# Kernel tuning notes

Measured on AMD Instinct MI355X. Metric: run time of the kernel, lower is better.

Reference implementation:

```python
import jax, jax.numpy as jnp
import numpy as np

B, S = 32, 128
VIDEO_SIZE, TITLE_SIZE = 768, 768
NUM_TAG, NUM_VOCAB, HIDDEN = 10000, 21128, 256


def setup_inputs() -> dict:
    key = jax.random.key(0)
    ks = jax.random.split(key, 10)
    video_feature = jax.random.normal(ks[0], (B, VIDEO_SIZE), dtype=jnp.float32)
    title_feature = jax.random.normal(ks[1], (B, S, TITLE_SIZE), dtype=jnp.float32)
    label_tag = jax.random.uniform(ks[2], (B, NUM_TAG), dtype=jnp.float32)
    label_mlm = jax.random.randint(ks[3], (B, S), 0, NUM_VOCAB, dtype=jnp.int64)
    Wt = jax.random.normal(ks[4], (NUM_TAG, VIDEO_SIZE), dtype=jnp.float32) * 0.02
    bt = jnp.zeros((NUM_TAG,), dtype=jnp.float32)
    Wm = jax.random.normal(ks[5], (NUM_VOCAB, TITLE_SIZE), dtype=jnp.float32) * 0.02
    bm = jnp.zeros((NUM_VOCAB,), dtype=jnp.float32)
    Wh = jax.random.normal(ks[6], (HIDDEN, VIDEO_SIZE + TITLE_SIZE), dtype=jnp.float32) * 0.02
    bh = jnp.zeros((HIDDEN,), dtype=jnp.float32)
    return {
        "video_feature": video_feature,
        "title_feature": title_feature,
        "label_tag": label_tag,
        "label_mlm": label_mlm,
        "Wt": Wt, "bt": bt, "Wm": Wm, "bm": bm, "Wh": Wh, "bh": bh,
    }


def reference(video_feature, title_feature, label_tag, label_mlm, Wt, bt, Wm, bm, Wh, bh):
    # tag head + BCEWithLogits (mean reduction), numerically stable form
    pred_tag = video_feature @ Wt.T + bt                       # [B, NUM_TAG]
    loss_tag = jnp.mean(
        jnp.maximum(pred_tag, 0.0) - pred_tag * label_tag
        + jnp.log1p(jnp.exp(-jnp.abs(pred_tag)))
    )
    pred_tag_sig = jax.nn.sigmoid(pred_tag)

    # mlm head: per-token vocab logits, masked CE summed over nonzero labels
    logits = jnp.einsum('bsd,vd->bsv', title_feature, Wm) + bm  # [B, S, V]
    lse = jax.nn.logsumexp(logits, axis=-1)                     # [B, S]
    gold = jnp.take_along_axis(logits, label_mlm[..., None], axis=-1)[..., 0]
    ce = lse - gold                                             # per-token NLL
    mask = (label_mlm != 0)
    loss_mlm = jnp.sum(jnp.where(mask, ce, 0.0))

    # fused embedding head + L2 normalize (torch eps 1e-12)
    feature = jnp.concatenate([video_feature, title_feature[:, 0]], axis=1)
    embedding = feature @ Wh.T + bh                             # [B, HIDDEN]
    norm = jnp.linalg.norm(embedding, axis=1, keepdims=True)
    normed_embedding = embedding / jnp.maximum(norm, 1e-12)

    return (pred_tag_sig, normed_embedding, loss_tag, loss_mlm)
```

## Files before the change

kernel.cpp:

```cpp
#include <hip/hip_runtime.h>
#include <hip/hip_bf16.h>
#include <math.h>

typedef short bf16x8 __attribute__((ext_vector_type(8)));
typedef float f32x4 __attribute__((ext_vector_type(4)));

#define KDIM 768
#define NTAG 10000
#define NVOC 21128
#define HID 256
#define NTOK 4096
#define NCHUNK 24
#define CHUNK 881
#define NTILE 28
#define TILEB 24576
#define M0 4.0f
#define WMSCALE 16.0f
#define INVSCALE 0.0625f
#define LOG2E 1.44269504f

#define WS_A     0ull
#define WS_PSUM  3145728ull
#define WS_GOLD  3538944ull
#define WS_TAGL  3555328ull
#define WS_WM8   3555392ull
#define WS_NEED  (WS_WM8 + 16515072ull + 65536ull)

#define OUT_EMB  320000
#define OUT_LTAG 328192
#define OUT_LMLM 328193

#define MLM_BLKS 768
#define TAG_BLKS 313
#define GOLD_BLKS 1024
#define EMB_BLKS 32
#define CONV_BLKS 1536
#define WMCV_BLKS (NCHUNK*NTILE)
#define TAIL_BLKS (TAG_BLKS + GOLD_BLKS + EMB_BLKS)

typedef const __attribute__((address_space(1))) unsigned int glds_g;
typedef __attribute__((address_space(3))) unsigned int glds_l;

static __device__ __forceinline__ unsigned short f2bf(float f) {
  unsigned u = __builtin_bit_cast(unsigned, f);
  u = u + 0x7FFFu + ((u >> 16) & 1u);
  return (unsigned short)(u >> 16);
}

static __device__ __forceinline__ int pk4_fp8(float4 v, float scale) {
  int w = __builtin_amdgcn_cvt_pk_fp8_f32(v.x * scale, v.y * scale, 0, false);
  w = __builtin_amdgcn_cvt_pk_fp8_f32(v.z * scale, v.w * scale, w, true);
  return w;
}

__global__ __launch_bounds__(256) void k_pre(
    const float* __restrict__ title, const float* __restrict__ video,
    const float* __restrict__ Wm,
    const float* __restrict__ Wt, const float* __restrict__ bt,
    const float* __restrict__ ylab, const int* __restrict__ lab,
    const float* __restrict__ bm,
    const float* __restrict__ Wh, const float* __restrict__ bh,
    char* __restrict__ A8, char* __restrict__ Wm8,
    float* __restrict__ out_sig, float* __restrict__ tagSum,
    float* __restrict__ gold, float* __restrict__ out_emb) {
  __shared__ __align__(1024) char smem[49664];
  const int bid = blockIdx.x, tid = threadIdx.x;
  const int wave = tid >> 6, lane = tid & 63, g = lane >> 4, col16 = lane & 15;

  if (bid < TAG_BLKS) {
    unsigned short* Bt = (unsigned short*)smem;
    float* wsum = (float*)(smem + 49152);
    #pragma unroll
    for (int j = 0; j < 12; ++j) {
      int sg = j * 256 + tid;
      int tt = (j >= 6) ? 1 : 0;
      int sgl = sg - tt * 1536;
      int kk = sgl >> 6, c = (sgl & 63) >> 2, gg = sgl & 3;
      int n = (bid * 2 + tt) * 16 + c;
      bf16x8 o = {};
      if (n < NTAG) {
        const float* wp = Wt + (size_t)n * KDIM + kk * 32 + gg * 8;
        float4 f0 = ((const float4*)wp)[0], f1 = ((const float4*)wp)[1];
        o[0] = (short)f2bf(f0.x); o[1] = (short)f2bf(f0.y);
        o[2] = (short)f2bf(f0.z); o[3] = (short)f2bf(f0.w);
        o[4] = (short)f2bf(f1.x); o[5] = (short)f2bf(f1.y);
        o[6] = (short)f2bf(f1.z); o[7] = (short)f2bf(f1.w);
      }
      *(bf16x8*)((char*)Bt + sg * 16) = o;
    }
    __syncthreads();

    const int ntile = bid * 2 + (wave >> 1), mhalf = wave & 1;
    float lacc = 0.f;
    if (ntile < 625) {
      bf16x8 a[24];
      const float* vrow = video + (size_t)(mhalf * 16 + col16) * KDIM;
      #pragma unroll
      for (int kk = 0; kk < 24; ++kk) {
        float4 f0 = *(const float4*)(vrow + kk * 32 + g * 8);
        float4 f1 = *(const float4*)(vrow + kk * 32 + g * 8 + 4);
        bf16x8 o;
        o[0] = (short)f2bf(f0.x); o[1] = (short)f2bf(f0.y);
        o[2] = (short)f2bf(f0.z); o[3] = (short)f2bf(f0.w);
        o[4] = (short)f2bf(f1.x); o[5] = (short)f2bf(f1.y);
        o[6] = (short)f2bf(f1.z); o[7] = (short)f2bf(f1.w);
        a[kk] = o;
      }
      const char* Bb = (const char*)Bt + (wave >> 1) * 24576 + col16 * 64 + g * 16;
      f32x4 acc = {0.f, 0.f, 0.f, 0.f};
      #pragma unroll
      for (int kk = 0; kk < 24; ++kk) {
        bf16x8 b = *(const bf16x8*)(Bb + kk * 1024);
        acc = __builtin_amdgcn_mfma_f32_16x16x32_bf16(a[kk], b, acc, 0, 0, 0);
      }
      const int nc = ntile * 16 + col16;
      if (nc < NTAG) {
        const float bias = bt[nc];
        #pragma unroll
        for (int rr = 0; rr < 4; ++rr) {
          int brow = mhalf * 16 + g * 4 + rr;
          float x = acc[rr] + bias;
          out_sig[(size_t)brow * NTAG + nc] = 1.f / (1.f + __expf(-x));
          float y = ylab[(size_t)brow * NTAG + nc];
          lacc += fmaxf(x, 0.f) - x * y + log1pf(__expf(-fabsf(x)));
        }
      }
    }
    #pragma unroll
    for (int m = 32; m; m >>= 1) lacc += __shfl_xor(lacc, m);
    if (lane == 0) wsum[wave] = lacc;
    __syncthreads();
    if (tid == 0) atomicAdd(tagSum, wsum[0] + wsum[1] + wsum[2] + wsum[3]);

  } else if (bid < TAG_BLKS + GOLD_BLKS) {
    int tok = (bid - TAG_BLKS) * 4 + wave;
    int l = lab[tok];
    float acc = 0.f;
    #pragma unroll
    for (int j = 0; j < 12; ++j) {
      int k = j * 64 + lane;
      acc += title[(size_t)tok * KDIM + k] * Wm[(size_t)l * KDIM + k];
    }
    #pragma unroll
    for (int m = 32; m; m >>= 1) acc += __shfl_xor(acc, m);
    if (lane == 0) gold[tok] = acc + bm[l];

  } else if (bid < TAIL_BLKS) {
    float* feat = (float*)smem;
    float* red = (float*)(smem + 49152);
    const int b = bid - TAG_BLKS - GOLD_BLKS;
    #pragma unroll
    for (int j = 0; j < 6; ++j) {
      int k = j * 256 + tid;
      feat[k] = (k < KDIM) ? video[(size_t)b * KDIM + k]
                           : title[(size_t)b * 128 * KDIM + (k - KDIM)];
    }
    __syncthreads();
    float acc = bh[tid];
    #pragma unroll 8
    for (int k = 0; k < 1536; k += 4) {
      float4 w = *(const float4*)(Wh + (size_t)tid * 1536 + k);
      acc += w.x * feat[k] + w.y * feat[k + 1] + w.z * feat[k + 2] + w.w * feat[k + 3];
    }
    float ss = acc * acc;
    #pragma unroll
    for (int m = 32; m; m >>= 1) ss += __shfl_xor(ss, m);
    if (lane == 0) red[wave] = ss;
    __syncthreads();
    float nrm = sqrtf(red[0] + red[1] + red[2] + red[3]);
    float scale = 1.f / fmaxf(nrm, 1e-12f);
    out_emb[(size_t)b * HID + tid] = acc * scale;

  } else if (bid < TAIL_BLKS + CONV_BLKS) {
    int i = (bid - TAIL_BLKS) * 256 + tid;
    float4 v0 = ((const float4*)title)[i * 2];
    float4 v1 = ((const float4*)title)[i * 2 + 1];
    int2 o = {pk4_fp8(v0, 1.f), pk4_fp8(v1, 1.f)};
    *(int2*)(A8 + (size_t)i * 8) = o;

  } else {
    char* tsm = smem;
    const int wblk = bid - TAIL_BLKS - CONV_BLKS;
    const int chunk = wblk / NTILE, tile = wblk % NTILE;
    const int n0 = chunk * CHUNK + tile * 32;
    const int nend = min(chunk * CHUNK + CHUNK, NVOC);
    #pragma unroll
    for (int j = 0; j < 12; ++j) {
      int p = j * 256 + tid;
      int r = p / 96, q = p % 96;
      int n = n0 + r;
      int2 o = {0, 0};
      if (n < nend) {
        const float* wp = Wm + (size_t)n * KDIM + q * 8;
        o.x = pk4_fp8(((const float4*)wp)[0], WMSCALE);
        o.y = pk4_fp8(((const float4*)wp)[1], WMSCALE);
      }
      *(int2*)(tsm + (q >> 2) * 1024 + (q & 3) * 256 + r * 8) = o;
    }
    __syncthreads();
    char* dst = Wm8 + (size_t)wblk * TILEB;
    #pragma unroll
    for (int j = 0; j < 6; ++j) {
      int idx = j * 256 + tid;
      *(int4*)(dst + idx * 16) = *(const int4*)(tsm + idx * 16);
    }
  }
}

template<bool WM8>
__global__ __launch_bounds__(256)
__attribute__((amdgpu_waves_per_eu(3, 3)))
void k_mlm(
    const char* __restrict__ A8,
    const float* __restrict__ Wm,
    const char* __restrict__ Wm8,
    const float* __restrict__ bm,
    float* __restrict__ psum) {
  __shared__ __align__(1024) char smem[2 * TILEB + 3584];
  char (*Bsm)[TILEB] = (char(*)[TILEB])smem;
  float* biasS = (float*)(smem + 2 * TILEB);
  const int tid = threadIdx.x;
  const int wave = tid >> 6, lane = tid & 63, g = lane >> 4, col = lane & 15;
  const int chunk = blockIdx.x % NCHUNK, mt = blockIdx.x / NCHUNK;
  const int nbeg = chunk * CHUNK;
  const int nend = min(nbeg + CHUNK, NVOC);

  for (int i = tid; i < NTILE * 32; i += 256) {
    int n = nbeg + i;
    biasS[i] = (n < nend) ? (bm[n] - M0) * LOG2E : -1e30f;
  }

  const int arow0 = mt * 128 + wave * 32;
  long a0[24], a1[24];
  #pragma unroll
  for (int kk = 0; kk < 24; ++kk) {
    a0[kk] = *(const long*)(A8 + (size_t)(arow0 + col) * KDIM + kk * 32 + g * 8);
    a1[kk] = *(const long*)(A8 + (size_t)(arow0 + 16 + col) * KDIM + kk * 32 + g * 8);
  }

  float s[8];
  #pragma unroll
  for (int i = 0; i < 8; ++i) s[i] = 0.f;

  const int off0 = col * 8 + g * 256;
  const float kinv = INVSCALE * LOG2E;

  auto COMPUTE = [&](int t) {
    const char* B = &Bsm[t & 1][0] + off0;
    f32x4 acc00 = {0.f,0.f,0.f,0.f}, acc10 = {0.f,0.f,0.f,0.f};
    f32x4 acc01 = {0.f,0.f,0.f,0.f}, acc11 = {0.f,0.f,0.f,0.f};
    #pragma unroll
    for (int kk = 0; kk < 24; ++kk) {
      long b0 = *(const long*)(B + kk * 1024);
      long b1 = *(const long*)(B + kk * 1024 + 128);
      acc00 = __builtin_amdgcn_mfma_f32_16x16x32_fp8_fp8(a0[kk], b0, acc00, 0, 0, 0);
      acc10 = __builtin_amdgcn_mfma_f32_16x16x32_fp8_fp8(a1[kk], b0, acc10, 0, 0, 0);
      acc01 = __builtin_amdgcn_mfma_f32_16x16x32_fp8_fp8(a0[kk], b1, acc01, 0, 0, 0);
      acc11 = __builtin_amdgcn_mfma_f32_16x16x32_fp8_fp8(a1[kk], b1, acc11, 0, 0, 0);
    }
    const float b20 = biasS[t * 32 + col];
    const float b21 = biasS[t * 32 + 16 + col];
    #pragma unroll
    for (int rr = 0; rr < 4; ++rr) {
      s[rr]     += exp2f(fmaf(acc00[rr], kinv, b20)) + exp2f(fmaf(acc01[rr], kinv, b21));
      s[rr + 4] += exp2f(fmaf(acc10[rr], kinv, b20)) + exp2f(fmaf(acc11[rr], kinv, b21));
    }
  };

  if constexpr (WM8) {
    const char* cbase = Wm8 + (size_t)chunk * NTILE * TILEB;
    auto STAGE = [&](int buf, int tt) {
      const char* src = cbase + (size_t)tt * TILEB + wave * 1024 + lane * 16;
      char* dst = &Bsm[buf][0] + wave * 1024;
      #pragma unroll
      for (int j = 0; j < 6; ++j) {
        __builtin_amdgcn_global_load_lds((glds_g*)(src + j * 4096),
                                         (glds_l*)(dst + j * 4096), 16, 0, 0);
      }
    };
    STAGE(0, 0);
    asm volatile("s_waitcnt lgkmcnt(0)" ::: "memory");
    __builtin_amdgcn_s_barrier();
    for (int t = 0; t < NTILE; ++t) {
      int tn = (t + 1 < NTILE) ? t + 1 : 0;
      STAGE((t + 1) & 1, tn);
      asm volatile("s_waitcnt vmcnt(6)" ::: "memory");
      __builtin_amdgcn_s_barrier();
      __builtin_amdgcn_sched_barrier(0);
      __builtin_amdgcn_s_setprio(1);
      COMPUTE(t);
      __builtin_amdgcn_s_setprio(0);
      __builtin_amdgcn_sched_barrier(0);
      __builtin_amdgcn_s_barrier();
    }
  } else {
    __syncthreads();
    for (int t = 0; t < NTILE; ++t) {
      #pragma unroll
      for (int j = 0; j < 6; ++j) {
        int sg = j * 256 + tid;
        int kk = sg >> 6, gg = (sg >> 4) & 3, nl0 = (sg & 15) * 2;
        int n_a = nbeg + t * 32 + nl0, n_b = n_a + 1;
        int4 o = {0, 0, 0, 0};
        if (n_a < nend) {
          const float* wp = Wm + (size_t)n_a * KDIM + kk * 32 + gg * 8;
          o.x = pk4_fp8(((const float4*)wp)[0], WMSCALE);
          o.y = pk4_fp8(((const float4*)wp)[1], WMSCALE);
        }
        if (n_b < nend) {
          const float* wp = Wm + (size_t)n_b * KDIM + kk * 32 + gg * 8;
          o.z = pk4_fp8(((const float4*)wp)[0], WMSCALE);
          o.w = pk4_fp8(((const float4*)wp)[1], WMSCALE);
        }
        *(int4*)(&Bsm[0][0] + kk * 1024 + gg * 256 + nl0 * 8) = o;
      }
      __syncthreads();
      COMPUTE(t);
      __syncthreads();
    }
  }

  #pragma unroll
  for (int i = 0; i < 8; ++i) {
    float v = s[i];
    v += __shfl_xor(v, 1);
    v += __shfl_xor(v, 2);
    v += __shfl_xor(v, 4);
    v += __shfl_xor(v, 8);
    s[i] = v;
  }
  if (col == 0) {
    #pragma unroll
    for (int mblk = 0; mblk < 2; ++mblk)
      #pragma unroll
      for (int rr = 0; rr < 4; ++rr) {
        int tok = arow0 + mblk * 16 + g * 4 + rr;
        psum[tok * NCHUNK + chunk] = s[mblk * 4 + rr];
      }
  }
}

__global__ __launch_bounds__(256) void k_final(
    const float* __restrict__ psum, const float* __restrict__ gold,
    const int* __restrict__ lab, const float* __restrict__ tagSum,
    float* __restrict__ out) {
  __shared__ float red[4];
  const int tid = threadIdx.x, wave = tid >> 6, lane = tid & 63;
  if (tid == 0) out[OUT_LTAG] = tagSum[0] / 320000.f;

  float lm = 0.f;
  for (int tok = tid; tok < NTOK; tok += 256) {
    float S = 0.f;
    #pragma unroll
    for (int c = 0; c < NCHUNK; ++c) S += psum[tok * NCHUNK + c];
    float lse = M0 + logf(S);
    if (lab[tok] != 0) lm += lse - gold[tok];
  }
  #pragma unroll
  for (int m = 32; m; m >>= 1) lm += __shfl_xor(lm, m);
  if (lane == 0) red[wave] = lm;
  __syncthreads();
  if (tid == 0) out[OUT_LMLM] = red[0] + red[1] + red[2] + red[3];
}

extern "C" void kernel_launch(void* const* d_in, const int* in_sizes, int n_in,
                              void* d_out, int out_size, void* d_ws, size_t ws_size,
                              hipStream_t stream) {
  const float* video = (const float*)d_in[0];
  const float* title = (const float*)d_in[1];
  const float* ylab  = (const float*)d_in[2];
  const int*   lab   = (const int*)d_in[3];
  const float* Wt = (const float*)d_in[4];
  const float* bt = (const float*)d_in[5];
  const float* Wm = (const float*)d_in[6];
  const float* bm = (const float*)d_in[7];
  const float* Wh = (const float*)d_in[8];
  const float* bh = (const float*)d_in[9];
  float* out = (float*)d_out;
  char* ws = (char*)d_ws;

  char* wsA8   = ws + WS_A;
  float* wsPsum = (float*)(ws + WS_PSUM);
  float* wsGold = (float*)(ws + WS_GOLD);
  float* wsTagl = (float*)(ws + WS_TAGL);
  char* wsWm8  = ws + WS_WM8;

  const bool useWm8 = ws_size >= WS_NEED;

  hipMemsetAsync(wsTagl, 0, 4, stream);
  k_pre<<<TAIL_BLKS + CONV_BLKS + WMCV_BLKS, 256, 0, stream>>>(
      title, video, Wm, Wt, bt, ylab, lab, bm, Wh, bh,
      wsA8, wsWm8, out, wsTagl, wsGold, out + OUT_EMB);
  if (useWm8)
    k_mlm<true><<<MLM_BLKS, 256, 0, stream>>>(wsA8, Wm, wsWm8, bm, wsPsum);
  else
    k_mlm<false><<<MLM_BLKS, 256, 0, stream>>>(wsA8, Wm, wsWm8, bm, wsPsum);
  k_final<<<1, 256, 0, stream>>>(wsPsum, wsGold, lab, wsTagl, out);
}
```

Baseline: 184.9 us.

## Overlap tag, gold and embedding heads with MLM GEMM in one interleaved kernel

Splits the prep kernel so that only the fp8 conversions of title and Wm run first, then merges the tag head, gold-logit gather and embedding head into the MLM kernel. Blocks are interleaved by role (3 of every 8 do MLM, 5 do tail work) so the independent small heads fill CUs alongside the long-running MLM blocks. It also makes the gold blocks process 16 tokens each instead of 4. The trade-off is a larger grid with many early-exit blocks. The shared-memory footprint and the waves-per-eu constraint now apply to the tail work too, which could limit how many blocks fit on a CU at once.

```diff
diff --git a/kernel.cpp b/kernel.cpp
--- a/kernel.cpp
+++ b/kernel.cpp
@@ -32,11 +32,12 @@
 
 #define MLM_BLKS 768
 #define TAG_BLKS 313
-#define GOLD_BLKS 1024
+#define GOLD_BLKS 256
 #define EMB_BLKS 32
+#define TAIL_JOBS (TAG_BLKS + GOLD_BLKS + EMB_BLKS)
+#define MAIN_GRID 2048
 #define CONV_BLKS 1536
 #define WMCV_BLKS (NCHUNK*NTILE)
-#define TAIL_BLKS (TAG_BLKS + GOLD_BLKS + EMB_BLKS)
 
 typedef const __attribute__((address_space(1))) unsigned int glds_g;
 typedef __attribute__((address_space(3))) unsigned int glds_l;
@@ -53,21 +54,194 @@
   return w;
 }
 
-__global__ __launch_bounds__(256) void k_pre(
-    const float* __restrict__ title, const float* __restrict__ video,
+__global__ __launch_bounds__(256) void k_conv(
+    const float* __restrict__ title, const float* __restrict__ Wm,
+    char* __restrict__ A8, char* __restrict__ Wm8) {
+  __shared__ __align__(1024) char tsm[TILEB];
+  const int bid = blockIdx.x, tid = threadIdx.x;
+  if (bid < CONV_BLKS) {
+    int i = bid * 256 + tid;
+    float4 v0 = ((const float4*)title)[i * 2];
+    float4 v1 = ((const float4*)title)[i * 2 + 1];
+    int2 o = {pk4_fp8(v0, 1.f), pk4_fp8(v1, 1.f)};
+    *(int2*)(A8 + (size_t)i * 8) = o;
+  } else {
+    const int wblk = bid - CONV_BLKS;
+    const int chunk = wblk / NTILE, tile = wblk % NTILE;
+    const int n0 = chunk * CHUNK + tile * 32;
+    const int nend = min(chunk * CHUNK + CHUNK, NVOC);
+    #pragma unroll
+    for (int j = 0; j < 12; ++j) {
+      int p = j * 256 + tid;
+      int r = p / 96, q = p % 96;
+      int n = n0 + r;
+      int2 o = {0, 0};
+      if (n < nend) {
+        const float* wp = Wm + (size_t)n * KDIM + q * 8;
+        o.x = pk4_fp8(((const float4*)wp)[0], WMSCALE);
+        o.y = pk4_fp8(((const float4*)wp)[1], WMSCALE);
+      }
+      *(int2*)(tsm + (q >> 2) * 1024 + (q & 3) * 256 + r * 8) = o;
+    }
+    __syncthreads();
+    char* dst = Wm8 + (size_t)wblk * TILEB;
+    #pragma unroll
+    for (int j = 0; j < 6; ++j) {
+      int idx = j * 256 + tid;
+      *(int4*)(dst + idx * 16) = *(const int4*)(tsm + idx * 16);
+    }
+  }
+}
+
+template<bool WM8>
+__global__ __launch_bounds__(256)
+__attribute__((amdgpu_waves_per_eu(3, 3)))
+void k_main(
+    const char* __restrict__ A8,
     const float* __restrict__ Wm,
+    const char* __restrict__ Wm8,
+    const float* __restrict__ bm,
+    float* __restrict__ psum,
+    const float* __restrict__ video, const float* __restrict__ title,
     const float* __restrict__ Wt, const float* __restrict__ bt,
     const float* __restrict__ ylab, const int* __restrict__ lab,
-    const float* __restrict__ bm,
     const float* __restrict__ Wh, const float* __restrict__ bh,
-    char* __restrict__ A8, char* __restrict__ Wm8,
     float* __restrict__ out_sig, float* __restrict__ tagSum,
     float* __restrict__ gold, float* __restrict__ out_emb) {
-  __shared__ __align__(1024) char smem[49664];
+  __shared__ __align__(1024) char smem[2 * TILEB + 3584];
   const int bid = blockIdx.x, tid = threadIdx.x;
-  const int wave = tid >> 6, lane = tid & 63, g = lane >> 4, col16 = lane & 15;
-
-  if (bid < TAG_BLKS) {
+  const int wave = tid >> 6, lane = tid & 63, g = lane >> 4, col = lane & 15;
+  const int role = bid & 7;
+
+  if (role < 3) {
+    const int mlm_idx = (bid >> 3) * 3 + role;
+    char (*Bsm)[TILEB] = (char(*)[TILEB])smem;
+    float* biasS = (float*)(smem + 2 * TILEB);
+    const int chunk = mlm_idx % NCHUNK, mt = mlm_idx / NCHUNK;
+    const int nbeg = chunk * CHUNK;
+    const int nend = min(nbeg + CHUNK, NVOC);
+
+    for (int i = tid; i < NTILE * 32; i += 256) {
+      int n = nbeg + i;
+      biasS[i] = (n < nend) ? (bm[n] - M0) * LOG2E : -1e30f;
+    }
+
+    const int arow0 = mt * 128 + wave * 32;
+    long a0[24], a1[24];
+    #pragma unroll
+    for (int kk = 0; kk < 24; ++kk) {
+      a0[kk] = *(const long*)(A8 + (size_t)(arow0 + col) * KDIM + kk * 32 + g * 8);
+      a1[kk] = *(const long*)(A8 + (size_t)(arow0 + 16 + col) * KDIM + kk * 32 + g * 8);
+    }
+
+    float s[8];
+    #pragma unroll
+    for (int i = 0; i < 8; ++i) s[i] = 0.f;
+
+    const int off0 = col * 8 + g * 256;
+    const float kinv = INVSCALE * LOG2E;
+
+    auto COMPUTE = [&](int t) {
+      const char* B = &Bsm[t & 1][0] + off0;
+      f32x4 acc00 = {0.f,0.f,0.f,0.f}, acc10 = {0.f,0.f,0.f,0.f};
+      f32x4 acc01 = {0.f,0.f,0.f,0.f}, acc11 = {0.f,0.f,0.f,0.f};
+      #pragma unroll
+      for (int kk = 0; kk < 24; ++kk) {
+        long b0 = *(const long*)(B + kk * 1024);
+        long b1 = *(const long*)(B + kk * 1024 + 128);
+        acc00 = __builtin_amdgcn_mfma_f32_16x16x32_fp8_fp8(a0[kk], b0, acc00, 0, 0, 0);
+        acc10 = __builtin_amdgcn_mfma_f32_16x16x32_fp8_fp8(a1[kk], b0, acc10, 0, 0, 0);
+        acc01 = __builtin_amdgcn_mfma_f32_16x16x32_fp8_fp8(a0[kk], b1, acc01, 0, 0, 0);
+        acc11 = __builtin_amdgcn_mfma_f32_16x16x32_fp8_fp8(a1[kk], b1, acc11, 0, 0, 0);
+      }
+      const float b20 = biasS[t * 32 + col];
+      const float b21 = biasS[t * 32 + 16 + col];
+      #pragma unroll
+      for (int rr = 0; rr < 4; ++rr) {
+        s[rr]     += exp2f(fmaf(acc00[rr], kinv, b20)) + exp2f(fmaf(acc01[rr], kinv, b21));
+        s[rr + 4] += exp2f(fmaf(acc10[rr], kinv, b20)) + exp2f(fmaf(acc11[rr], kinv, b21));
+      }
+    };
+
+    if constexpr (WM8) {
+      const char* cbase = Wm8 + (size_t)chunk * NTILE * TILEB;
+      auto STAGE = [&](int buf, int tt) {
+        const char* src = cbase + (size_t)tt * TILEB + wave * 1024 + lane * 16;
+        char* dst = &Bsm[buf][0] + wave * 1024;
+        #pragma unroll
+        for (int j = 0; j < 6; ++j) {
+          __builtin_amdgcn_global_load_lds((glds_g*)(src + j * 4096),
+                                           (glds_l*)(dst + j * 4096), 16, 0, 0);
+        }
+      };
+      STAGE(0, 0);
+      asm volatile("s_waitcnt lgkmcnt(0)" ::: "memory");
+      __builtin_amdgcn_s_barrier();
+      for (int t = 0; t < NTILE; ++t) {
+        int tn = (t + 1 < NTILE) ? t + 1 : 0;
+        STAGE((t + 1) & 1, tn);
+        asm volatile("s_waitcnt vmcnt(6)" ::: "memory");
+        __builtin_amdgcn_s_barrier();
+        __builtin_amdgcn_sched_barrier(0);
+        __builtin_amdgcn_s_setprio(1);
+        COMPUTE(t);
+        __builtin_amdgcn_s_setprio(0);
+        __builtin_amdgcn_sched_barrier(0);
+        __builtin_amdgcn_s_barrier();
+      }
+    } else {
+      __syncthreads();
+      for (int t = 0; t < NTILE; ++t) {
+        #pragma unroll
+        for (int j = 0; j < 6; ++j) {
+          int sg = j * 256 + tid;
+          int kk = sg >> 6, gg = (sg >> 4) & 3, nl0 = (sg & 15) * 2;
+          int n_a = nbeg + t * 32 + nl0, n_b = n_a + 1;
+          int4 o = {0, 0, 0, 0};
+          if (n_a < nend) {
+            const float* wp = Wm + (size_t)n_a * KDIM + kk * 32 + gg * 8;
+            o.x = pk4_fp8(((const float4*)wp)[0], WMSCALE);
+            o.y = pk4_fp8(((const float4*)wp)[1], WMSCALE);
+          }
+          if (n_b < nend) {
+            const float* wp = Wm + (size_t)n_b * KDIM + kk * 32 + gg * 8;
+            o.z = pk4_fp8(((const float4*)wp)[0], WMSCALE);
+            o.w = pk4_fp8(((const float4*)wp)[1], WMSCALE);
+          }
+          *(int4*)(&Bsm[0][0] + kk * 1024 + gg * 256 + nl0 * 8) = o;
+        }
+        __syncthreads();
+        COMPUTE(t);
+        __syncthreads();
+      }
+    }
+
+    #pragma unroll
+    for (int i = 0; i < 8; ++i) {
+      float v = s[i];
+      v += __shfl_xor(v, 1);
+      v += __shfl_xor(v, 2);
+      v += __shfl_xor(v, 4);
+      v += __shfl_xor(v, 8);
+      s[i] = v;
+    }
+    if (col == 0) {
+      #pragma unroll
+      for (int mblk = 0; mblk < 2; ++mblk)
+        #pragma unroll
+        for (int rr = 0; rr < 4; ++rr) {
+          int tok = arow0 + mblk * 16 + g * 4 + rr;
+          psum[tok * NCHUNK + chunk] = s[mblk * 4 + rr];
+        }
+    }
+    return;
+  }
+
+  const int tail_idx = (bid >> 3) * 5 + (role - 3);
+  if (tail_idx >= TAIL_JOBS) return;
+
+  if (tail_idx < TAG_BLKS) {
+    const int tb = tail_idx;
     unsigned short* Bt = (unsigned short*)smem;
     float* wsum = (float*)(smem + 49152);
     #pragma unroll
@@ -76,7 +250,7 @@
       int tt = (j >= 6) ? 1 : 0;
       int sgl = sg - tt * 1536;
       int kk = sgl >> 6, c = (sgl & 63) >> 2, gg = sgl & 3;
-      int n = (bid * 2 + tt) * 16 + c;
+      int n = (tb * 2 + tt) * 16 + c;
       bf16x8 o = {};
       if (n < NTAG) {
         const float* wp = Wt + (size_t)n * KDIM + kk * 32 + gg * 8;
@@ -90,11 +264,11 @@
     }
     __syncthreads();
 
-    const int ntile = bid * 2 + (wave >> 1), mhalf = wave & 1;
+    const int ntile = tb * 2 + (wave >> 1), mhalf = wave & 1;
     float lacc = 0.f;
     if (ntile < 625) {
       bf16x8 a[24];
-      const float* vrow = video + (size_t)(mhalf * 16 + col16) * KDIM;
+      const float* vrow = video + (size_t)(mhalf * 16 + col) * KDIM;
       #pragma unroll
       for (int kk = 0; kk < 24; ++kk) {
         float4 f0 = *(const float4*)(vrow + kk * 32 + g * 8);
@@ -106,14 +280,14 @@
         o[6] = (short)f2bf(f1.z); o[7] = (short)f2bf(f1.w);
         a[kk] = o;
       }
-      const char* Bb = (const char*)Bt + (wave >> 1) * 24576 + col16 * 64 + g * 16;
+      const char* Bb = (const char*)Bt + (wave >> 1) * 24576 + col * 64 + g * 16;
       f32x4 acc = {0.f, 0.f, 0.f, 0.f};
       #pragma unroll
       for (int kk = 0; kk < 24; ++kk) {
         bf16x8 b = *(const bf16x8*)(Bb + kk * 1024);
         acc = __builtin_amdgcn_mfma_f32_16x16x32_bf16(a[kk], b, acc, 0, 0, 0);
       }
-      const int nc = ntile * 16 + col16;
+      const int nc = ntile * 16 + col;
       if (nc < NTAG) {
         const float bias = bt[nc];
         #pragma unroll
@@ -132,23 +306,27 @@
     __syncthreads();
     if (tid == 0) atomicAdd(tagSum, wsum[0] + wsum[1] + wsum[2] + wsum[3]);
 
-  } else if (bid < TAG_BLKS + GOLD_BLKS) {
-    int tok = (bid - TAG_BLKS) * 4 + wave;
-    int l = lab[tok];
-    float acc = 0.f;
-    #pragma unroll
-    for (int j = 0; j < 12; ++j) {
-      int k = j * 64 + lane;
-      acc += title[(size_t)tok * KDIM + k] * Wm[(size_t)l * KDIM + k];
-    }
-    #pragma unroll
-    for (int m = 32; m; m >>= 1) acc += __shfl_xor(acc, m);
-    if (lane == 0) gold[tok] = acc + bm[l];
-
-  } else if (bid < TAIL_BLKS) {
+  } else if (tail_idx < TAG_BLKS + GOLD_BLKS) {
+    const int tbase = (tail_idx - TAG_BLKS) * 16;
+    #pragma unroll
+    for (int u = 0; u < 4; ++u) {
+      int tok = tbase + wave * 4 + u;
+      int l = lab[tok];
+      float acc = 0.f;
+      #pragma unroll
+      for (int j = 0; j < 12; ++j) {
+        int k = j * 64 + lane;
+        acc += title[(size_t)tok * KDIM + k] * Wm[(size_t)l * KDIM + k];
+      }
+      #pragma unroll
+      for (int m = 32; m; m >>= 1) acc += __shfl_xor(acc, m);
+      if (lane == 0) gold[tok] = acc + bm[l];
+    }
+
+  } else {
     float* feat = (float*)smem;
     float* red = (float*)(smem + 49152);
-    const int b = bid - TAG_BLKS - GOLD_BLKS;
+    const int b = tail_idx - TAG_BLKS - GOLD_BLKS;
     #pragma unroll
     for (int j = 0; j < 6; ++j) {
       int k = j * 256 + tid;
@@ -170,173 +348,6 @@
     float nrm = sqrtf(red[0] + red[1] + red[2] + red[3]);
     float scale = 1.f / fmaxf(nrm, 1e-12f);
     out_emb[(size_t)b * HID + tid] = acc * scale;
-
-  } else if (bid < TAIL_BLKS + CONV_BLKS) {
-    int i = (bid - TAIL_BLKS) * 256 + tid;
-    float4 v0 = ((const float4*)title)[i * 2];
-    float4 v1 = ((const float4*)title)[i * 2 + 1];
-    int2 o = {pk4_fp8(v0, 1.f), pk4_fp8(v1, 1.f)};
-    *(int2*)(A8 + (size_t)i * 8) = o;
-
-  } else {
-    char* tsm = smem;
-    const int wblk = bid - TAIL_BLKS - CONV_BLKS;
-    const int chunk = wblk / NTILE, tile = wblk % NTILE;
-    const int n0 = chunk * CHUNK + tile * 32;
-    const int nend = min(chunk * CHUNK + CHUNK, NVOC);
-    #pragma unroll
-    for (int j = 0; j < 12; ++j) {
-      int p = j * 256 + tid;
-      int r = p / 96, q = p % 96;
-      int n = n0 + r;
-      int2 o = {0, 0};
-      if (n < nend) {
-        const float* wp = Wm + (size_t)n * KDIM + q * 8;
-        o.x = pk4_fp8(((const float4*)wp)[0], WMSCALE);
-        o.y = pk4_fp8(((const float4*)wp)[1], WMSCALE);
-      }
-      *(int2*)(tsm + (q >> 2) * 1024 + (q & 3) * 256 + r * 8) = o;
-    }
-    __syncthreads();
-    char* dst = Wm8 + (size_t)wblk * TILEB;
-    #pragma unroll
-    for (int j = 0; j < 6; ++j) {
-      int idx = j * 256 + tid;
-      *(int4*)(dst + idx * 16) = *(const int4*)(tsm + idx * 16);
-    }
-  }
-}
-
-template<bool WM8>
-__global__ __launch_bounds__(256)
-__attribute__((amdgpu_waves_per_eu(3, 3)))
-void k_mlm(
-    const char* __restrict__ A8,
-    const float* __restrict__ Wm,
-    const char* __restrict__ Wm8,
-    const float* __restrict__ bm,
-    float* __restrict__ psum) {
-  __shared__ __align__(1024) char smem[2 * TILEB + 3584];
-  char (*Bsm)[TILEB] = (char(*)[TILEB])smem;
-  float* biasS = (float*)(smem + 2 * TILEB);
-  const int tid = threadIdx.x;
-  const int wave = tid >> 6, lane = tid & 63, g = lane >> 4, col = lane & 15;
-  const int chunk = blockIdx.x % NCHUNK, mt = blockIdx.x / NCHUNK;
-  const int nbeg = chunk * CHUNK;
-  const int nend = min(nbeg + CHUNK, NVOC);
-
-  for (int i = tid; i < NTILE * 32; i += 256) {
-    int n = nbeg + i;
-    biasS[i] = (n < nend) ? (bm[n] - M0) * LOG2E : -1e30f;
-  }
-
-  const int arow0 = mt * 128 + wave * 32;
-  long a0[24], a1[24];
-  #pragma unroll
-  for (int kk = 0; kk < 24; ++kk) {
-    a0[kk] = *(const long*)(A8 + (size_t)(arow0 + col) * KDIM + kk * 32 + g * 8);
-    a1[kk] = *(const long*)(A8 + (size_t)(arow0 + 16 + col) * KDIM + kk * 32 + g * 8);
-  }
-
-  float s[8];
-  #pragma unroll
-  for (int i = 0; i < 8; ++i) s[i] = 0.f;
-
-  const int off0 = col * 8 + g * 256;
-  const float kinv = INVSCALE * LOG2E;
-
-  auto COMPUTE = [&](int t) {
-    const char* B = &Bsm[t & 1][0] + off0;
-    f32x4 acc00 = {0.f,0.f,0.f,0.f}, acc10 = {0.f,0.f,0.f,0.f};
-    f32x4 acc01 = {0.f,0.f,0.f,0.f}, acc11 = {0.f,0.f,0.f,0.f};
-    #pragma unroll
-    for (int kk = 0; kk < 24; ++kk) {
-      long b0 = *(const long*)(B + kk * 1024);
-      long b1 = *(const long*)(B + kk * 1024 + 128);
-      acc00 = __builtin_amdgcn_mfma_f32_16x16x32_fp8_fp8(a0[kk], b0, acc00, 0, 0, 0);
-      acc10 = __builtin_amdgcn_mfma_f32_16x16x32_fp8_fp8(a1[kk], b0, acc10, 0, 0, 0);
-      acc01 = __builtin_amdgcn_mfma_f32_16x16x32_fp8_fp8(a0[kk], b1, acc01, 0, 0, 0);
-      acc11 = __builtin_amdgcn_mfma_f32_16x16x32_fp8_fp8(a1[kk], b1, acc11, 0, 0, 0);
-    }
-    const float b20 = biasS[t * 32 + col];
-    const float b21 = biasS[t * 32 + 16 + col];
-    #pragma unroll
-    for (int rr = 0; rr < 4; ++rr) {
-      s[rr]     += exp2f(fmaf(acc00[rr], kinv, b20)) + exp2f(fmaf(acc01[rr], kinv, b21));
-      s[rr + 4] += exp2f(fmaf(acc10[rr], kinv, b20)) + exp2f(fmaf(acc11[rr], kinv, b21));
-    }
-  };
-
-  if constexpr (WM8) {
-    const char* cbase = Wm8 + (size_t)chunk * NTILE * TILEB;
-    auto STAGE = [&](int buf, int tt) {
-      const char* src = cbase + (size_t)tt * TILEB + wave * 1024 + lane * 16;
-      char* dst = &Bsm[buf][0] + wave * 1024;
-      #pragma unroll
-      for (int j = 0; j < 6; ++j) {
-        __builtin_amdgcn_global_load_lds((glds_g*)(src + j * 4096),
-                                         (glds_l*)(dst + j * 4096), 16, 0, 0);
-      }
-    };
-    STAGE(0, 0);
-    asm volatile("s_waitcnt lgkmcnt(0)" ::: "memory");
-    __builtin_amdgcn_s_barrier();
-    for (int t = 0; t < NTILE; ++t) {
-      int tn = (t + 1 < NTILE) ? t + 1 : 0;
-      STAGE((t + 1) & 1, tn);
-      asm volatile("s_waitcnt vmcnt(6)" ::: "memory");
-      __builtin_amdgcn_s_barrier();
-      __builtin_amdgcn_sched_barrier(0);
-      __builtin_amdgcn_s_setprio(1);
-      COMPUTE(t);
-      __builtin_amdgcn_s_setprio(0);
-      __builtin_amdgcn_sched_barrier(0);
-      __builtin_amdgcn_s_barrier();
-    }
-  } else {
-    __syncthreads();
-    for (int t = 0; t < NTILE; ++t) {
-      #pragma unroll
-      for (int j = 0; j < 6; ++j) {
-        int sg = j * 256 + tid;
-        int kk = sg >> 6, gg = (sg >> 4) & 3, nl0 = (sg & 15) * 2;
-        int n_a = nbeg + t * 32 + nl0, n_b = n_a + 1;
-        int4 o = {0, 0, 0, 0};
-        if (n_a < nend) {
-          const float* wp = Wm + (size_t)n_a * KDIM + kk * 32 + gg * 8;
-          o.x = pk4_fp8(((const float4*)wp)[0], WMSCALE);
-          o.y = pk4_fp8(((const float4*)wp)[1], WMSCALE);
-        }
-        if (n_b < nend) {
-          const float* wp = Wm + (size_t)n_b * KDIM + kk * 32 + gg * 8;
-          o.z = pk4_fp8(((const float4*)wp)[0], WMSCALE);
-          o.w = pk4_fp8(((const float4*)wp)[1], WMSCALE);
-        }
-        *(int4*)(&Bsm[0][0] + kk * 1024 + gg * 256 + nl0 * 8) = o;
-      }
-      __syncthreads();
-      COMPUTE(t);
-      __syncthreads();
-    }
-  }
-
-  #pragma unroll
-  for (int i = 0; i < 8; ++i) {
-    float v = s[i];
-    v += __shfl_xor(v, 1);
-    v += __shfl_xor(v, 2);
-    v += __shfl_xor(v, 4);
-    v += __shfl_xor(v, 8);
-    s[i] = v;
-  }
-  if (col == 0) {
-    #pragma unroll
-    for (int mblk = 0; mblk < 2; ++mblk)
-      #pragma unroll
-      for (int rr = 0; rr < 4; ++rr) {
-        int tok = arow0 + mblk * 16 + g * 4 + rr;
-        psum[tok * NCHUNK + chunk] = s[mblk * 4 + rr];
-      }
   }
 }
 
@@ -388,12 +399,14 @@
   const bool useWm8 = ws_size >= WS_NEED;
 
   hipMemsetAsync(wsTagl, 0, 4, stream);
-  k_pre<<<TAIL_BLKS + CONV_BLKS + WMCV_BLKS, 256, 0, stream>>>(
-      title, video, Wm, Wt, bt, ylab, lab, bm, Wh, bh,
-      wsA8, wsWm8, out, wsTagl, wsGold, out + OUT_EMB);
+  k_conv<<<CONV_BLKS + WMCV_BLKS, 256, 0, stream>>>(title, Wm, wsA8, wsWm8);
   if (useWm8)
-    k_mlm<true><<<MLM_BLKS, 256, 0, stream>>>(wsA8, Wm, wsWm8, bm, wsPsum);
+    k_main<true><<<MAIN_GRID, 256, 0, stream>>>(
+        wsA8, Wm, wsWm8, bm, wsPsum, video, title, Wt, bt, ylab, lab,
+        Wh, bh, out, wsTagl, wsGold, out + OUT_EMB);
   else
-    k_mlm<false><<<MLM_BLKS, 256, 0, stream>>>(wsA8, Wm, wsWm8, bm, wsPsum);
+    k_main<false><<<MAIN_GRID, 256, 0, stream>>>(
+        wsA8, Wm, wsWm8, bm, wsPsum, video, title, Wt, bt, ylab, lab,
+        Wh, bh, out, wsTagl, wsGold, out + OUT_EMB);
   k_final<<<1, 256, 0, stream>>>(wsPsum, wsGold, lab, wsTagl, out);
 }
```

After: 270.0 us. 1.46x slower.

## Split preprocessing kernel into conversion and tail kernels with smaller LDS

Applied to the files above, without the earlier changes.

The monolithic prologue kernel is split into k_conv, which handles the fp8 conversion of title and Wm and uses only 24KB of LDS, and k_tail, which handles the tag head, gold logits and embedding and runs after the MLM kernel. The tag blocks now cover one 16-column tile each, with 625 blocks and half the LDS, so occupancy improves. The MLM kernel can start once conversion finishes instead of waiting for the tag, gold and embedding work. This adds one more kernel launch, and in the tag blocks only two of the four waves do MFMA work.

```diff
diff --git a/kernel.cpp b/kernel.cpp
--- a/kernel.cpp
+++ b/kernel.cpp
@@ -31,12 +31,12 @@
 #define OUT_LMLM 328193
 
 #define MLM_BLKS 768
-#define TAG_BLKS 313
+#define TAG_BLKS 625
 #define GOLD_BLKS 1024
 #define EMB_BLKS 32
+#define TAIL_GRID (TAG_BLKS + GOLD_BLKS + EMB_BLKS)
 #define CONV_BLKS 1536
 #define WMCV_BLKS (NCHUNK*NTILE)
-#define TAIL_BLKS (TAG_BLKS + GOLD_BLKS + EMB_BLKS)
 
 typedef const __attribute__((address_space(1))) unsigned int glds_g;
 typedef __attribute__((address_space(3))) unsigned int glds_l;
@@ -53,134 +53,28 @@
   return w;
 }
 
-__global__ __launch_bounds__(256) void k_pre(
-    const float* __restrict__ title, const float* __restrict__ video,
-    const float* __restrict__ Wm,
-    const float* __restrict__ Wt, const float* __restrict__ bt,
-    const float* __restrict__ ylab, const int* __restrict__ lab,
-    const float* __restrict__ bm,
-    const float* __restrict__ Wh, const float* __restrict__ bh,
-    char* __restrict__ A8, char* __restrict__ Wm8,
-    float* __restrict__ out_sig, float* __restrict__ tagSum,
-    float* __restrict__ gold, float* __restrict__ out_emb) {
-  __shared__ __align__(1024) char smem[49664];
+static __device__ __forceinline__ bf16x8 cvt8(float4 f0, float4 f1) {
+  bf16x8 o;
+  o[0] = (short)f2bf(f0.x); o[1] = (short)f2bf(f0.y);
+  o[2] = (short)f2bf(f0.z); o[3] = (short)f2bf(f0.w);
+  o[4] = (short)f2bf(f1.x); o[5] = (short)f2bf(f1.y);
+  o[6] = (short)f2bf(f1.z); o[7] = (short)f2bf(f1.w);
+  return o;
+}
+
+__global__ __launch_bounds__(256) void k_conv(
+    const float* __restrict__ title, const float* __restrict__ Wm,
+    char* __restrict__ A8, char* __restrict__ Wm8) {
+  __shared__ __align__(1024) char tsm[TILEB];
   const int bid = blockIdx.x, tid = threadIdx.x;
-  const int wave = tid >> 6, lane = tid & 63, g = lane >> 4, col16 = lane & 15;
-
-  if (bid < TAG_BLKS) {
-    unsigned short* Bt = (unsigned short*)smem;
-    float* wsum = (float*)(smem + 49152);
-    #pragma unroll
-    for (int j = 0; j < 12; ++j) {
-      int sg = j * 256 + tid;
-      int tt = (j >= 6) ? 1 : 0;
-      int sgl = sg - tt * 1536;
-      int kk = sgl >> 6, c = (sgl & 63) >> 2, gg = sgl & 3;
-      int n = (bid * 2 + tt) * 16 + c;
-      bf16x8 o = {};
-      if (n < NTAG) {
-        const float* wp = Wt + (size_t)n * KDIM + kk * 32 + gg * 8;
-        float4 f0 = ((const float4*)wp)[0], f1 = ((const float4*)wp)[1];
-        o[0] = (short)f2bf(f0.x); o[1] = (short)f2bf(f0.y);
-        o[2] = (short)f2bf(f0.z); o[3] = (short)f2bf(f0.w);
-        o[4] = (short)f2bf(f1.x); o[5] = (short)f2bf(f1.y);
-        o[6] = (short)f2bf(f1.z); o[7] = (short)f2bf(f1.w);
-      }
-      *(bf16x8*)((char*)Bt + sg * 16) = o;
-    }
-    __syncthreads();
-
-    const int ntile = bid * 2 + (wave >> 1), mhalf = wave & 1;
-    float lacc = 0.f;
-    if (ntile < 625) {
-      bf16x8 a[24];
-      const float* vrow = video + (size_t)(mhalf * 16 + col16) * KDIM;
-      #pragma unroll
-      for (int kk = 0; kk < 24; ++kk) {
-        float4 f0 = *(const float4*)(vrow + kk * 32 + g * 8);
-        float4 f1 = *(const float4*)(vrow + kk * 32 + g * 8 + 4);
-        bf16x8 o;
-        o[0] = (short)f2bf(f0.x); o[1] = (short)f2bf(f0.y);
-        o[2] = (short)f2bf(f0.z); o[3] = (short)f2bf(f0.w);
-        o[4] = (short)f2bf(f1.x); o[5] = (short)f2bf(f1.y);
-        o[6] = (short)f2bf(f1.z); o[7] = (short)f2bf(f1.w);
-        a[kk] = o;
-      }
-      const char* Bb = (const char*)Bt + (wave >> 1) * 24576 + col16 * 64 + g * 16;
-      f32x4 acc = {0.f, 0.f, 0.f, 0.f};
-      #pragma unroll
-      for (int kk = 0; kk < 24; ++kk) {
-        bf16x8 b = *(const bf16x8*)(Bb + kk * 1024);
-        acc = __builtin_amdgcn_mfma_f32_16x16x32_bf16(a[kk], b, acc, 0, 0, 0);
-      }
-      const int nc = ntile * 16 + col16;
-      if (nc < NTAG) {
-        const float bias = bt[nc];
-        #pragma unroll
-        for (int rr = 0; rr < 4; ++rr) {
-          int brow = mhalf * 16 + g * 4 + rr;
-          float x = acc[rr] + bias;
-          out_sig[(size_t)brow * NTAG + nc] = 1.f / (1.f + __expf(-x));
-          float y = ylab[(size_t)brow * NTAG + nc];
-          lacc += fmaxf(x, 0.f) - x * y + log1pf(__expf(-fabsf(x)));
-        }
-      }
-    }
-    #pragma unroll
-    for (int m = 32; m; m >>= 1) lacc += __shfl_xor(lacc, m);
-    if (lane == 0) wsum[wave] = lacc;
-    __syncthreads();
-    if (tid == 0) atomicAdd(tagSum, wsum[0] + wsum[1] + wsum[2] + wsum[3]);
-
-  } else if (bid < TAG_BLKS + GOLD_BLKS) {
-    int tok = (bid - TAG_BLKS) * 4 + wave;
-    int l = lab[tok];
-    float acc = 0.f;
-    #pragma unroll
-    for (int j = 0; j < 12; ++j) {
-      int k = j * 64 + lane;
-      acc += title[(size_t)tok * KDIM + k] * Wm[(size_t)l * KDIM + k];
-    }
-    #pragma unroll
-    for (int m = 32; m; m >>= 1) acc += __shfl_xor(acc, m);
-    if (lane == 0) gold[tok] = acc + bm[l];
-
-  } else if (bid < TAIL_BLKS) {
-    float* feat = (float*)smem;
-    float* red = (float*)(smem + 49152);
-    const int b = bid - TAG_BLKS - GOLD_BLKS;
-    #pragma unroll
-    for (int j = 0; j < 6; ++j) {
-      int k = j * 256 + tid;
-      feat[k] = (k < KDIM) ? video[(size_t)b * KDIM + k]
-                           : title[(size_t)b * 128 * KDIM + (k - KDIM)];
-    }
-    __syncthreads();
-    float acc = bh[tid];
-    #pragma unroll 8
-    for (int k = 0; k < 1536; k += 4) {
-      float4 w = *(const float4*)(Wh + (size_t)tid * 1536 + k);
-      acc += w.x * feat[k] + w.y * feat[k + 1] + w.z * feat[k + 2] + w.w * feat[k + 3];
-    }
-    float ss = acc * acc;
-    #pragma unroll
-    for (int m = 32; m; m >>= 1) ss += __shfl_xor(ss, m);
-    if (lane == 0) red[wave] = ss;
-    __syncthreads();
-    float nrm = sqrtf(red[0] + red[1] + red[2] + red[3]);
-    float scale = 1.f / fmaxf(nrm, 1e-12f);
-    out_emb[(size_t)b * HID + tid] = acc * scale;
-
-  } else if (bid < TAIL_BLKS + CONV_BLKS) {
-    int i = (bid - TAIL_BLKS) * 256 + tid;
+  if (bid < CONV_BLKS) {
+    int i = bid * 256 + tid;
     float4 v0 = ((const float4*)title)[i * 2];
     float4 v1 = ((const float4*)title)[i * 2 + 1];
     int2 o = {pk4_fp8(v0, 1.f), pk4_fp8(v1, 1.f)};
     *(int2*)(A8 + (size_t)i * 8) = o;
-
   } else {
-    char* tsm = smem;
-    const int wblk = bid - TAIL_BLKS - CONV_BLKS;
+    const int wblk = bid - CONV_BLKS;
     const int chunk = wblk / NTILE, tile = wblk % NTILE;
     const int n0 = chunk * CHUNK + tile * 32;
     const int nend = min(chunk * CHUNK + CHUNK, NVOC);
@@ -340,6 +234,112 @@
   }
 }
 
+__global__ __launch_bounds__(256) void k_tail(
+    const float* __restrict__ video, const float* __restrict__ title,
+    const float* __restrict__ Wt, const float* __restrict__ bt,
+    const float* __restrict__ ylab, const int* __restrict__ lab,
+    const float* __restrict__ Wm, const float* __restrict__ bm,
+    const float* __restrict__ Wh, const float* __restrict__ bh,
+    float* __restrict__ out_sig, float* __restrict__ tagSum,
+    float* __restrict__ gold, float* __restrict__ out_emb) {
+  __shared__ __align__(64) char smem[24640];
+  const int bid = blockIdx.x, tid = threadIdx.x;
+  const int wave = tid >> 6, lane = tid & 63, g = lane >> 4, col = lane & 15;
+
+  if (bid < TAG_BLKS) {
+    unsigned short* Bt = (unsigned short*)smem;
+    float* wsum = (float*)(smem + 24576);
+    #pragma unroll
+    for (int j = 0; j < 6; ++j) {
+      int sg = j * 256 + tid;
+      int kk = sg >> 6, c = (sg & 63) >> 2, gg = sg & 3;
+      int n = bid * 16 + c;
+      bf16x8 o = {};
+      if (n < NTAG) {
+        const float* wp = Wt + (size_t)n * KDIM + kk * 32 + gg * 8;
+        o = cvt8(((const float4*)wp)[0], ((const float4*)wp)[1]);
+      }
+      *(bf16x8*)((char*)Bt + sg * 16) = o;
+    }
+    __syncthreads();
+
+    float lacc = 0.f;
+    if (wave < 2) {
+      const int mhalf = wave;
+      bf16x8 a[24];
+      const float* vrow = video + (size_t)(mhalf * 16 + col) * KDIM;
+      #pragma unroll
+      for (int kk = 0; kk < 24; ++kk) {
+        a[kk] = cvt8(*(const float4*)(vrow + kk * 32 + g * 8),
+                     *(const float4*)(vrow + kk * 32 + g * 8 + 4));
+      }
+      const char* Bb = (const char*)Bt + col * 64 + g * 16;
+      f32x4 acc = {0.f, 0.f, 0.f, 0.f};
+      #pragma unroll
+      for (int kk = 0; kk < 24; ++kk) {
+        bf16x8 b = *(const bf16x8*)(Bb + kk * 1024);
+        acc = __builtin_amdgcn_mfma_f32_16x16x32_bf16(a[kk], b, acc, 0, 0, 0);
+      }
+      const int nc = bid * 16 + col;
+      if (nc < NTAG) {
+        const float bias = bt[nc];
+        #pragma unroll
+        for (int rr = 0; rr < 4; ++rr) {
+          int brow = mhalf * 16 + g * 4 + rr;
+          float x = acc[rr] + bias;
+          out_sig[(size_t)brow * NTAG + nc] = 1.f / (1.f + __expf(-x));
+          float y = ylab[(size_t)brow * NTAG + nc];
+          lacc += fmaxf(x, 0.f) - x * y + log1pf(__expf(-fabsf(x)));
+        }
+      }
+      #pragma unroll
+      for (int m = 32; m; m >>= 1) lacc += __shfl_xor(lacc, m);
+      if (lane == 0) wsum[wave] = lacc;
+    }
+    __syncthreads();
+    if (tid == 0) atomicAdd(tagSum, wsum[0] + wsum[1]);
+
+  } else if (bid < TAG_BLKS + GOLD_BLKS) {
+    int tok = (bid - TAG_BLKS) * 4 + wave;
+    int l = lab[tok];
+    float acc = 0.f;
+    #pragma unroll
+    for (int j = 0; j < 12; ++j) {
+      int k = j * 64 + lane;
+      acc += title[(size_t)tok * KDIM + k] * Wm[(size_t)l * KDIM + k];
+    }
+    #pragma unroll
+    for (int m = 32; m; m >>= 1) acc += __shfl_xor(acc, m);
+    if (lane == 0) gold[tok] = acc + bm[l];
+
+  } else {
+    float* feat = (float*)smem;
+    float* red = (float*)(smem + 6144);
+    const int b = bid - TAG_BLKS - GOLD_BLKS;
+    #pragma unroll
+    for (int j = 0; j < 6; ++j) {
+      int k = j * 256 + tid;
+      feat[k] = (k < KDIM) ? video[(size_t)b * KDIM + k]
+                           : title[(size_t)b * 128 * KDIM + (k - KDIM)];
+    }
+    __syncthreads();
+    float acc = bh[tid];
+    #pragma unroll 8
+    for (int k = 0; k < 1536; k += 4) {
+      float4 w = *(const float4*)(Wh + (size_t)tid * 1536 + k);
+      acc += w.x * feat[k] + w.y * feat[k + 1] + w.z * feat[k + 2] + w.w * feat[k + 3];
+    }
+    float ss = acc * acc;
+    #pragma unroll
+    for (int m = 32; m; m >>= 1) ss += __shfl_xor(ss, m);
+    if (lane == 0) red[wave] = ss;
+    __syncthreads();
+    float nrm = sqrtf(red[0] + red[1] + red[2] + red[3]);
+    float scale = 1.f / fmaxf(nrm, 1e-12f);
+    out_emb[(size_t)b * HID + tid] = acc * scale;
+  }
+}
+
 __global__ __launch_bounds__(256) void k_final(
     const float* __restrict__ psum, const float* __restrict__ gold,
     const int* __restrict__ lab, const float* __restrict__ tagSum,
@@ -388,12 +388,13 @@
   const bool useWm8 = ws_size >= WS_NEED;
 
   hipMemsetAsync(wsTagl, 0, 4, stream);
-  k_pre<<<TAIL_BLKS + CONV_BLKS + WMCV_BLKS, 256, 0, stream>>>(
-      title, video, Wm, Wt, bt, ylab, lab, bm, Wh, bh,
-      wsA8, wsWm8, out, wsTagl, wsGold, out + OUT_EMB);
+  k_conv<<<CONV_BLKS + WMCV_BLKS, 256, 0, stream>>>(title, Wm, wsA8, wsWm8);
   if (useWm8)
     k_mlm<true><<<MLM_BLKS, 256, 0, stream>>>(wsA8, Wm, wsWm8, bm, wsPsum);
   else
     k_mlm<false><<<MLM_BLKS, 256, 0, stream>>>(wsA8, Wm, wsWm8, bm, wsPsum);
+  k_tail<<<TAIL_GRID, 256, 0, stream>>>(
+      video, title, Wt, bt, ylab, lab, Wm, bm, Wh, bh,
+      out, wsTagl, wsGold, out + OUT_EMB);
   k_final<<<1, 256, 0, stream>>>(wsPsum, wsGold, lab, wsTagl, out);
 }
```

After: 197.5 us. +6.8%, slower.
